# Performance work log

Hardware: AMD Instinct MI355X
Metric: run time of the kernel (lower is better)

## Reference

```python
import jax, jax.numpy as jnp
import numpy as np

B_, S_, F_ = 4096, 512, 3
MAT_PTS = 128
N_OUT = 3
N_LAT = MAT_PTS * N_OUT  # 384
E, NU = 3130.0, 0.3
A_H, B_H, C_H = 64.8, 33.6, 0.003407
MU = E / (2.0 * (1.0 + NU))
LAM = E * NU / ((1.0 + NU) * (1.0 - 2.0 * NU))
NEWTON_ITERS = 12
VEC1 = jnp.array([1.0, 1.0, 1.0, 0.0], dtype=jnp.float32)  # identity in Voigt-4 (xx,yy,zz,xy)


def setup_inputs() -> dict:
    key = jax.random.key(0)
    k1, k2, k3 = jax.random.split(key, 3)
    x = jax.random.normal(k1, (B_, S_, F_), dtype=jnp.float32) * 0.01
    W1 = jax.random.normal(k2, (N_LAT, F_), dtype=jnp.float32) * (1.0 / np.sqrt(F_))
    W2 = jax.random.normal(k3, (N_OUT, N_LAT), dtype=jnp.float32) * (1.0 / np.sqrt(N_LAT))
    return {"x": x, "W1": W1, "W2": W2}


def _j2_update(state, eps):
    """J2 plane-strain return mapping with exponential hardening.
    state: (ep [N,4] tensorial plastic strain, kappa [N] eq. plastic strain)
    eps:   [N,3] engineering strain (exx, eyy, gxy).
    Returns new state and stress [N,3] (sxx, syy, sxy)."""
    ep, kappa = state
    e = jnp.stack([eps[:, 0], eps[:, 1], jnp.zeros_like(eps[:, 0]), 0.5 * eps[:, 2]], axis=-1)
    ee = e - ep                                   # elastic strain, tensorial
    tr = ee[:, 0] + ee[:, 1] + ee[:, 2]
    sig = 2.0 * MU * ee + LAM * tr[:, None] * VEC1  # trial stress (xx,yy,zz,xy)
    p = (sig[:, 0] + sig[:, 1] + sig[:, 2]) / 3.0
    s = sig - p[:, None] * VEC1                    # deviatoric
    q = jnp.sqrt(1.5 * (s[:, 0] ** 2 + s[:, 1] ** 2 + s[:, 2] ** 2 + 2.0 * s[:, 3] ** 2))
    sy = A_H - B_H * jnp.exp(-kappa / C_H)
    f = q - sy                                     # yield function (trial)

    def newton_step(dg, _):
        kp = kappa + dg
        r = q - 3.0 * MU * dg - (A_H - B_H * jnp.exp(-kp / C_H))
        dr = -3.0 * MU - (B_H / C_H) * jnp.exp(-kp / C_H)
        dg_new = jnp.maximum(dg - r / dr, 0.0)
        return dg_new, None

    dg0 = jnp.zeros_like(q)
    dg, _ = jax.lax.scan(newton_step, dg0, None, length=NEWTON_ITERS)
    dg = jnp.where(f > 0.0, dg, 0.0)
    q_safe = jnp.maximum(q, 1e-12)
    n = 1.5 * s / q_safe[:, None]                  # flow direction
    sig_new = sig - 2.0 * MU * dg[:, None] * n
    ep_new = ep + dg[:, None] * n
    kappa_new = kappa + dg
    stress = jnp.stack([sig_new[:, 0], sig_new[:, 1], sig_new[:, 3]], axis=-1)
    return (ep_new, kappa_new), stress


def _forward(x, W1, W2):
    B, S, F = x.shape
    N = B * MAT_PTS  # material points across the batch
    # fc1 is time-independent: apply to all timesteps at once
    h = jnp.einsum('bsf,lf->bsl', x, W1)                 # [B,S,n_latents]
    eps_seq = h.reshape(B, S, MAT_PTS, F_).transpose(1, 0, 2, 3).reshape(S, N, F_)
    ep0 = jnp.zeros((N, 4), dtype=x.dtype)
    k0 = jnp.zeros((N,), dtype=x.dtype)
    _, stresses = jax.lax.scan(_j2_update, (ep0, k0), eps_seq)  # [S,N,3]
    lat = stresses.reshape(S, B, N_LAT).transpose(1, 0, 2)      # [B,S,n_latents]
    return jnp.einsum('bsl,ol->bso', lat, W2)                   # [B,S,n_outputs]


def reference(x, W1, W2):
    return _forward(x, W1, W2)
```

## Files before the change

kernel.cpp:

```cpp
#include <hip/hip_runtime.h>
#include <math.h>

#define S_LEN 512
#define CH 8
#define NSEG 128
#define TBL_L0 -22.0f
#define TBL_INVH 4.0f
#define TBL_H 0.25f

typedef float v2f __attribute__((ext_vector_type(2)));

__device__ __forceinline__ float fast_rcp(float x) { return __builtin_amdgcn_rcpf(x); }
__device__ __forceinline__ float fast_rsq(float x) { return __builtin_amdgcn_rsqf(x); }
__device__ __forceinline__ float exp2s(float x)    { return __builtin_amdgcn_exp2f(x); }
__device__ __forceinline__ v2f rsqv(v2f a)  { return (v2f){fast_rsq(a.x), fast_rsq(a.y)}; }
__device__ __forceinline__ v2f minv(v2f a, v2f b) { return __builtin_elementwise_min(a, b); }
__device__ __forceinline__ v2f vfma(v2f a, v2f b, v2f c) {
    return (v2f){ __builtin_fmaf(a.x, b.x, c.x), __builtin_fmaf(a.y, b.y, c.y) };
}

template <int CTRL>
__device__ __forceinline__ float dpp_add(float v) {
    int vi = __builtin_bit_cast(int, v);
    int t  = __builtin_amdgcn_update_dpp(vi, vi, CTRL, 0xF, 0xF, true);
    return v + __builtin_bit_cast(float, t);
}

__global__ __launch_bounds__(128, 4) void prnn_kernel(
    const float* __restrict__ x,
    const float* __restrict__ W1,
    const float* __restrict__ W2,
    float* __restrict__ out)
{
    const double MUd = 3130.0 / 2.6;
    const double Cd  = 0.003407;
    const double K2d = 1.4426950408889634 / Cd;
    const double S3  = 1.7320508075688772;
    const float MU      = (float)MUd;
    const float MUS3    = (float)(MUd * S3);
    const float CP      = (float)(7825.0 / 3.0);
    const float AH      = 64.8f;
    const float TMC     = (float)(3.0 * MUd * Cd);
    const float MQ      = (float)(-K2d / (3.0 * MUd));
    const float KA0     = (float)(1.4492898 + (64.8 / (3.0 * MUd)) * K2d);
    const float I3      = (float)(1.0 / 3.0);
    const float IS3     = (float)(1.0 / S3);
    const float LOG2E   = 1.4426950408889634f;
    const float LN08    = (float)(0.8 * 0.6931471805599453);

    const int tid  = threadIdx.x;
    const int lane = tid & 63;
    const int wv   = tid >> 6;
    const int b    = blockIdx.x * 2 + wv;

    __shared__ float2 xs01[2][S_LEN];
    __shared__ float  xs2g[2][S_LEN];
    __shared__ float  part[2][CH][3][17];
    __shared__ float2 wtab[NSEG];

    {
        float wn = 0.0f;
        if (tid <= NSEG) {
            const float sarg = TBL_L0 + (float)tid * TBL_H;
            const float z = exp2s(sarg);
            float w = fmaxf(LN08 * sarg, z * (1.0f - z));
            #pragma unroll
            for (int it = 0; it < 4; ++it) {
                const float y   = exp2s(w * LOG2E);
                const float g   = w * y;
                const float F   = g - z;
                const float Fp  = g + y;
                const float den = Fp*Fp - 0.5f*((F*y)*(2.0f + w));
                w = w - (F*Fp)*fast_rcp(den);
            }
            wn = w;
            ((float*)wtab)[tid] = wn;
        }
        __syncthreads();
        float wnext = 0.0f;
        if (tid < NSEG) wnext = ((float*)wtab)[tid + 1];
        __syncthreads();
        if (tid < NSEG) {
            const float sl = -TMC * (wnext - wn) * TBL_INVH;
            const float bi = (AH - TMC * wn) - sl * (TBL_L0 + (float)tid * TBL_H);
            wtab[tid] = (float2){sl, bi};
        }
        __syncthreads();
    }

    v2f P[3], Mr[3], T3[3], pv[3];
    #pragma unroll
    for (int f = 0; f < 3; ++f) {
        const int mA = lane, mB = lane + 64;
        v2f av = (v2f){ W1[(mA*3 + 0)*3 + f], W1[(mB*3 + 0)*3 + f] };
        v2f bv = (v2f){ W1[(mA*3 + 1)*3 + f], W1[(mB*3 + 1)*3 + f] };
        v2f cv = (v2f){ W1[(mA*3 + 2)*3 + f], W1[(mB*3 + 2)*3 + f] };
        P[f]  = MU*(av + bv);
        Mr[f] = MUS3*(av - bv);
        T3[f] = MUS3*cv;
        pv[f] = CP*(av + bv);
    }
    v2f wp[3], wm[3], w3[3];
    float w2raw[2][3][2];
    float gsel0, gsel1, gsel2;
    {
        float G[3][3];
        #pragma unroll
        for (int o = 0; o < 3; ++o) {
            v2f w0 = (v2f){ W2[o*384 + lane*3 + 0], W2[o*384 + (lane+64)*3 + 0] };
            v2f w1 = (v2f){ W2[o*384 + lane*3 + 1], W2[o*384 + (lane+64)*3 + 1] };
            v2f wsh= (v2f){ W2[o*384 + lane*3 + 2], W2[o*384 + (lane+64)*3 + 2] };
            wp[o] = I3 *(w0 + w1);
            wm[o] = IS3*(w0 - w1);
            w3[o] = IS3*wsh;
            v2f ws = w0 + w1;
            #pragma unroll
            for (int f = 0; f < 3; ++f) {
                v2f gv = ws * pv[f];
                float g = gv.x + gv.y;
                #pragma unroll
                for (int mm = 1; mm < 64; mm <<= 1) g += __shfl_xor(g, mm, 64);
                G[o][f] = g;
            }
        }
        const int ro = lane % 3;
        gsel0 = (ro == 0) ? G[0][0] : (ro == 1) ? G[1][0] : G[2][0];
        gsel1 = (ro == 0) ? G[0][1] : (ro == 1) ? G[1][1] : G[2][1];
        gsel2 = (ro == 0) ? G[0][2] : (ro == 1) ? G[1][2] : G[2][2];
    }

    const float* xb = x + (size_t)b * (S_LEN*3);
    for (int i = lane; i < S_LEN; i += 64) {
        const float c0 = xb[i*3 + 0], c1 = xb[i*3 + 1], c2 = xb[i*3 + 2];
        float p0 = 0.f, p1 = 0.f, p2 = 0.f;
        if (i > 0) { p0 = xb[i*3 - 3]; p1 = xb[i*3 - 2]; p2 = xb[i*3 - 1]; }
        xs01[wv][i] = (float2){ c0 - p0, c1 - p1 };
        xs2g[wv][i] = c2 - p2;
    }

    v2f sp = (v2f){0.f,0.f}, sm = sp, s3 = sp;
    v2f ka2 = (v2f){KA0, KA0};
    float* outb = out + (size_t)b * (S_LEN*3);
    const int rtt0 = (lane < 24) ? (lane / 3) : 0;

    #pragma unroll 1
    for (int tc = 0; tc < S_LEN; tc += CH) {
        const float* xrow = xb + (size_t)(tc + rtt0)*3;
        const float fx0 = xrow[0], fx1 = xrow[1], fx2 = xrow[2];

        #pragma unroll
        for (int tt = 0; tt < CH; ++tt) {
            const int t = tc + tt;
            const float2 dx01 = xs01[wv][t];
            const float  dx2  = xs2g[wv][t];
            const float dx0 = dx01.x, dx1 = dx01.y;

            v2f p  = P[0]*dx0 + P[1]*dx1 + P[2]*dx2 + sp;
            v2f m  = Mr[0]*dx0 + Mr[1]*dx1 + Mr[2]*dx2 + sm;
            v2f d3 = T3[0]*dx0 + T3[1]*dx1 + T3[2]*dx2 + s3;

            v2f h = vfma(p, p, vfma(m, m, vfma(d3, d3, (v2f){1e-24f,1e-24f})));
            v2f qi = rsqv(h);
            v2f q  = h * qi;

            v2f g   = q * MQ;
            v2f l2z = g + ka2;
            const float fix = __builtin_fmaf(l2z.x, TBL_INVH, -TBL_L0*TBL_INVH);
            const float fiy = __builtin_fmaf(l2z.y, TBL_INVH, -TBL_L0*TBL_INVH);
            const unsigned ix = (unsigned)fix;
            const unsigned iy = (unsigned)fiy;
            const float2 tx = wtab[ix];
            const float2 ty = wtab[iy];
            v2f sv = (v2f){ __builtin_fmaf(tx.x, l2z.x, tx.y),
                            __builtin_fmaf(ty.x, l2z.y, ty.y) };
            v2f u   = minv(sv*qi, (v2f){1.0f,1.0f});
            ka2 = vfma(-u, g, l2z);

            sp = u*p; sm = u*m; s3 = u*d3;

            v2f a0 = wp[0]*sp + wm[0]*sm + w3[0]*s3;
            v2f a1 = wp[1]*sp + wm[1]*sm + w3[1]*s3;
            v2f a2 = wp[2]*sp + wm[2]*sm + w3[2]*s3;
            float c0 = a0.x + a0.y;
            float c1 = a1.x + a1.y;
            float c2 = a2.x + a2.y;

            c0 = dpp_add<0xB1>(c0); c0 = dpp_add<0x4E>(c0);
            c1 = dpp_add<0xB1>(c1); c1 = dpp_add<0x4E>(c1);
            c2 = dpp_add<0xB1>(c2); c2 = dpp_add<0x4E>(c2);
            if ((lane & 3) == 0) {
                const int g16 = lane >> 2;
                part[wv][tt][0][g16] = c0;
                part[wv][tt][1][g16] = c1;
                part[wv][tt][2][g16] = c2;
            }
        }
        if (lane < 24) {
            const int rtt = lane / 3, ro = lane - rtt*3;
            const float4* pp = (const float4*)&part[wv][rtt][ro][0];
            const float4 v0 = pp[0], v1 = pp[1], v2v = pp[2], v3 = pp[3];
            float s = ((v0.x + v0.y) + (v0.z + v0.w))
                    + ((v1.x + v1.y) + (v1.z + v1.w))
                    + ((v2v.x + v2v.y) + (v2v.z + v2v.w))
                    + ((v3.x + v3.y) + (v3.z + v3.w));
            s = __builtin_fmaf(gsel0, fx0, s);
            s = __builtin_fmaf(gsel1, fx1, s);
            s = __builtin_fmaf(gsel2, fx2, s);
            outb[tc*3 + lane] = s;
        }
    }
}

extern "C" void kernel_launch(void* const* d_in, const int* in_sizes, int n_in,
                              void* d_out, int out_size, void* d_ws, size_t ws_size,
                              hipStream_t stream) {
    const float* x  = (const float*)d_in[0];
    const float* W1 = (const float*)d_in[1];
    const float* W2 = (const float*)d_in[2];
    float* out = (float*)d_out;
    prnn_kernel<<<2048, 128, 0, stream>>>(x, W1, W2, out);
}
```

Before: 275.5 us.

## Split each batch across two waves, one material point per lane

Before, each wave handled one batch element with two material points per lane. Now a 128-thread block handles one batch element, one point per thread, across 4096 blocks. The two waves' partial reductions are combined through shared memory with block barriers every chunk of timesteps. The lookup table is shrunk and shifted, and launch bounds are raised to allow more resident blocks. This halves the serial per-lane work and doubles parallelism, but adds two __syncthreads per chunk and loses the two-point ILP per lane.

```diff
diff --git a/kernel.cpp b/kernel.cpp
--- a/kernel.cpp
+++ b/kernel.cpp
@@ -3,21 +3,14 @@
 
 #define S_LEN 512
 #define CH 8
-#define NSEG 128
-#define TBL_L0 -22.0f
+#define NSEG 97
+#define TBL_L0 -15.0f
 #define TBL_INVH 4.0f
 #define TBL_H 0.25f
-
-typedef float v2f __attribute__((ext_vector_type(2)));
 
 __device__ __forceinline__ float fast_rcp(float x) { return __builtin_amdgcn_rcpf(x); }
 __device__ __forceinline__ float fast_rsq(float x) { return __builtin_amdgcn_rsqf(x); }
 __device__ __forceinline__ float exp2s(float x)    { return __builtin_amdgcn_exp2f(x); }
-__device__ __forceinline__ v2f rsqv(v2f a)  { return (v2f){fast_rsq(a.x), fast_rsq(a.y)}; }
-__device__ __forceinline__ v2f minv(v2f a, v2f b) { return __builtin_elementwise_min(a, b); }
-__device__ __forceinline__ v2f vfma(v2f a, v2f b, v2f c) {
-    return (v2f){ __builtin_fmaf(a.x, b.x, c.x), __builtin_fmaf(a.y, b.y, c.y) };
-}
 
 template <int CTRL>
 __device__ __forceinline__ float dpp_add(float v) {
@@ -26,7 +19,7 @@
     return v + __builtin_bit_cast(float, t);
 }
 
-__global__ __launch_bounds__(128, 4) void prnn_kernel(
+__global__ __launch_bounds__(128, 6) void prnn_kernel(
     const float* __restrict__ x,
     const float* __restrict__ W1,
     const float* __restrict__ W2,
@@ -51,11 +44,11 @@
     const int tid  = threadIdx.x;
     const int lane = tid & 63;
     const int wv   = tid >> 6;
-    const int b    = blockIdx.x * 2 + wv;
-
-    __shared__ float2 xs01[2][S_LEN];
-    __shared__ float  xs2g[2][S_LEN];
-    __shared__ float  part[2][CH][3][17];
+    const int b    = blockIdx.x;
+
+    __shared__ float2 xs01[S_LEN];
+    __shared__ float  xs2g[S_LEN];
+    __shared__ float  part[2][CH][3][16];
     __shared__ float2 wtab[NSEG];
 
     {
@@ -85,105 +78,111 @@
             const float bi = (AH - TMC * wn) - sl * (TBL_L0 + (float)tid * TBL_H);
             wtab[tid] = (float2){sl, bi};
         }
-        __syncthreads();
-    }
-
-    v2f P[3], Mr[3], T3[3], pv[3];
+    }
+
+    float P[3], Mr[3], T3[3], pvr[3];
     #pragma unroll
     for (int f = 0; f < 3; ++f) {
-        const int mA = lane, mB = lane + 64;
-        v2f av = (v2f){ W1[(mA*3 + 0)*3 + f], W1[(mB*3 + 0)*3 + f] };
-        v2f bv = (v2f){ W1[(mA*3 + 1)*3 + f], W1[(mB*3 + 1)*3 + f] };
-        v2f cv = (v2f){ W1[(mA*3 + 2)*3 + f], W1[(mB*3 + 2)*3 + f] };
-        P[f]  = MU*(av + bv);
-        Mr[f] = MUS3*(av - bv);
-        T3[f] = MUS3*cv;
-        pv[f] = CP*(av + bv);
-    }
-    v2f wp[3], wm[3], w3[3];
-    float w2raw[2][3][2];
-    float gsel0, gsel1, gsel2;
+        const float av = W1[(tid*3 + 0)*3 + f];
+        const float bv = W1[(tid*3 + 1)*3 + f];
+        const float cv = W1[(tid*3 + 2)*3 + f];
+        P[f]   = MU*(av + bv);
+        Mr[f]  = MUS3*(av - bv);
+        T3[f]  = MUS3*cv;
+        pvr[f] = CP*(av + bv);
+    }
+    float wp[3], wm[3], w3[3], ws[3];
+    #pragma unroll
+    for (int o = 0; o < 3; ++o) {
+        const float w0  = W2[o*384 + tid*3 + 0];
+        const float w1  = W2[o*384 + tid*3 + 1];
+        const float wsh = W2[o*384 + tid*3 + 2];
+        wp[o] = I3 *(w0 + w1);
+        wm[o] = IS3*(w0 - w1);
+        w3[o] = IS3*wsh;
+        ws[o] = w0 + w1;
+    }
+
+    float gsel0 = 0.f, gsel1 = 0.f, gsel2 = 0.f;
     {
-        float G[3][3];
         #pragma unroll
-        for (int o = 0; o < 3; ++o) {
-            v2f w0 = (v2f){ W2[o*384 + lane*3 + 0], W2[o*384 + (lane+64)*3 + 0] };
-            v2f w1 = (v2f){ W2[o*384 + lane*3 + 1], W2[o*384 + (lane+64)*3 + 1] };
-            v2f wsh= (v2f){ W2[o*384 + lane*3 + 2], W2[o*384 + (lane+64)*3 + 2] };
-            wp[o] = I3 *(w0 + w1);
-            wm[o] = IS3*(w0 - w1);
-            w3[o] = IS3*wsh;
-            v2f ws = w0 + w1;
+        for (int o = 0; o < 3; ++o)
             #pragma unroll
             for (int f = 0; f < 3; ++f) {
-                v2f gv = ws * pv[f];
-                float g = gv.x + gv.y;
+                float g = ws[o] * pvr[f];
                 #pragma unroll
                 for (int mm = 1; mm < 64; mm <<= 1) g += __shfl_xor(g, mm, 64);
-                G[o][f] = g;
-            }
-        }
-        const int ro = lane % 3;
-        gsel0 = (ro == 0) ? G[0][0] : (ro == 1) ? G[1][0] : G[2][0];
-        gsel1 = (ro == 0) ? G[0][1] : (ro == 1) ? G[1][1] : G[2][1];
-        gsel2 = (ro == 0) ? G[0][2] : (ro == 1) ? G[1][2] : G[2][2];
+                if (lane == 0) part[wv][0][o][f] = g;
+            }
+        __syncthreads();
+        if (tid < 24) {
+            const int ro = tid % 3;
+            gsel0 = part[0][0][ro][0] + part[1][0][ro][0];
+            gsel1 = part[0][0][ro][1] + part[1][0][ro][1];
+            gsel2 = part[0][0][ro][2] + part[1][0][ro][2];
+        }
+        __syncthreads();
     }
 
     const float* xb = x + (size_t)b * (S_LEN*3);
-    for (int i = lane; i < S_LEN; i += 64) {
+    for (int i = tid; i < S_LEN; i += 128) {
         const float c0 = xb[i*3 + 0], c1 = xb[i*3 + 1], c2 = xb[i*3 + 2];
         float p0 = 0.f, p1 = 0.f, p2 = 0.f;
         if (i > 0) { p0 = xb[i*3 - 3]; p1 = xb[i*3 - 2]; p2 = xb[i*3 - 1]; }
-        xs01[wv][i] = (float2){ c0 - p0, c1 - p1 };
-        xs2g[wv][i] = c2 - p2;
-    }
-
-    v2f sp = (v2f){0.f,0.f}, sm = sp, s3 = sp;
-    v2f ka2 = (v2f){KA0, KA0};
+        xs01[i] = (float2){ c0 - p0, c1 - p1 };
+        xs2g[i] = c2 - p2;
+    }
+    __syncthreads();
+
+    float sp = 0.f, sm = 0.f, s3 = 0.f, ka2 = KA0;
     float* outb = out + (size_t)b * (S_LEN*3);
-    const int rtt0 = (lane < 24) ? (lane / 3) : 0;
+    const int rtt0 = (tid < 24) ? (tid / 3) : 0;
 
     #pragma unroll 1
     for (int tc = 0; tc < S_LEN; tc += CH) {
-        const float* xrow = xb + (size_t)(tc + rtt0)*3;
-        const float fx0 = xrow[0], fx1 = xrow[1], fx2 = xrow[2];
+        float fx0 = 0.f, fx1 = 0.f, fx2 = 0.f;
+        if (tid < 24) {
+            const float* xrow = xb + (size_t)(tc + rtt0)*3;
+            fx0 = xrow[0]; fx1 = xrow[1]; fx2 = xrow[2];
+        }
 
         #pragma unroll
         for (int tt = 0; tt < CH; ++tt) {
             const int t = tc + tt;
-            const float2 dx01 = xs01[wv][t];
-            const float  dx2  = xs2g[wv][t];
+            const float2 dx01 = xs01[t];
+            const float  dx2  = xs2g[t];
             const float dx0 = dx01.x, dx1 = dx01.y;
 
-            v2f p  = P[0]*dx0 + P[1]*dx1 + P[2]*dx2 + sp;
-            v2f m  = Mr[0]*dx0 + Mr[1]*dx1 + Mr[2]*dx2 + sm;
-            v2f d3 = T3[0]*dx0 + T3[1]*dx1 + T3[2]*dx2 + s3;
-
-            v2f h = vfma(p, p, vfma(m, m, vfma(d3, d3, (v2f){1e-24f,1e-24f})));
-            v2f qi = rsqv(h);
-            v2f q  = h * qi;
-
-            v2f g   = q * MQ;
-            v2f l2z = g + ka2;
-            const float fix = __builtin_fmaf(l2z.x, TBL_INVH, -TBL_L0*TBL_INVH);
-            const float fiy = __builtin_fmaf(l2z.y, TBL_INVH, -TBL_L0*TBL_INVH);
-            const unsigned ix = (unsigned)fix;
-            const unsigned iy = (unsigned)fiy;
-            const float2 tx = wtab[ix];
-            const float2 ty = wtab[iy];
-            v2f sv = (v2f){ __builtin_fmaf(tx.x, l2z.x, tx.y),
-                            __builtin_fmaf(ty.x, l2z.y, ty.y) };
-            v2f u   = minv(sv*qi, (v2f){1.0f,1.0f});
-            ka2 = vfma(-u, g, l2z);
+            const float p  = __builtin_fmaf(P[0], dx0,
+                              __builtin_fmaf(P[1], dx1,
+                              __builtin_fmaf(P[2], dx2, sp)));
+            const float m  = __builtin_fmaf(Mr[0], dx0,
+                              __builtin_fmaf(Mr[1], dx1,
+                              __builtin_fmaf(Mr[2], dx2, sm)));
+            const float d3 = __builtin_fmaf(T3[0], dx0,
+                              __builtin_fmaf(T3[1], dx1,
+                              __builtin_fmaf(T3[2], dx2, s3)));
+
+            const float h  = __builtin_fmaf(p, p,
+                              __builtin_fmaf(m, m,
+                              __builtin_fmaf(d3, d3, 1e-24f)));
+            const float qi = fast_rsq(h);
+            const float q  = h * qi;
+
+            const float g   = q * MQ;
+            const float l2z = g + ka2;
+            const float fi  = __builtin_fmaf(l2z, TBL_INVH, -TBL_L0*TBL_INVH);
+            const unsigned ii = (unsigned)fi;
+            const float2 tb = wtab[ii];
+            const float sv  = __builtin_fmaf(tb.x, l2z, tb.y);
+            const float u   = fminf(sv*qi, 1.0f);
+            ka2 = __builtin_fmaf(-u, g, l2z);
 
             sp = u*p; sm = u*m; s3 = u*d3;
 
-            v2f a0 = wp[0]*sp + wm[0]*sm + w3[0]*s3;
-            v2f a1 = wp[1]*sp + wm[1]*sm + w3[1]*s3;
-            v2f a2 = wp[2]*sp + wm[2]*sm + w3[2]*s3;
-            float c0 = a0.x + a0.y;
-            float c1 = a1.x + a1.y;
-            float c2 = a2.x + a2.y;
+            float c0 = __builtin_fmaf(wp[0], sp, __builtin_fmaf(wm[0], sm, w3[0]*s3));
+            float c1 = __builtin_fmaf(wp[1], sp, __builtin_fmaf(wm[1], sm, w3[1]*s3));
+            float c2 = __builtin_fmaf(wp[2], sp, __builtin_fmaf(wm[2], sm, w3[2]*s3));
 
             c0 = dpp_add<0xB1>(c0); c0 = dpp_add<0x4E>(c0);
             c1 = dpp_add<0xB1>(c1); c1 = dpp_add<0x4E>(c1);
@@ -195,19 +194,24 @@
                 part[wv][tt][2][g16] = c2;
             }
         }
-        if (lane < 24) {
-            const int rtt = lane / 3, ro = lane - rtt*3;
-            const float4* pp = (const float4*)&part[wv][rtt][ro][0];
-            const float4 v0 = pp[0], v1 = pp[1], v2v = pp[2], v3 = pp[3];
-            float s = ((v0.x + v0.y) + (v0.z + v0.w))
-                    + ((v1.x + v1.y) + (v1.z + v1.w))
-                    + ((v2v.x + v2v.y) + (v2v.z + v2v.w))
-                    + ((v3.x + v3.y) + (v3.z + v3.w));
+        __syncthreads();
+        if (tid < 24) {
+            const int rtt = tid / 3, ro = tid - rtt*3;
+            const float4* p0 = (const float4*)&part[0][rtt][ro][0];
+            const float4* p1 = (const float4*)&part[1][rtt][ro][0];
+            float s = 0.0f;
+            #pragma unroll
+            for (int k = 0; k < 4; ++k) {
+                const float4 va = p0[k], vb = p1[k];
+                s += ((va.x + va.y) + (va.z + va.w))
+                   + ((vb.x + vb.y) + (vb.z + vb.w));
+            }
             s = __builtin_fmaf(gsel0, fx0, s);
             s = __builtin_fmaf(gsel1, fx1, s);
             s = __builtin_fmaf(gsel2, fx2, s);
-            outb[tc*3 + lane] = s;
-        }
+            outb[tc*3 + tid] = s;
+        }
+        __syncthreads();
     }
 }
 
@@ -218,5 +222,5 @@
     const float* W1 = (const float*)d_in[1];
     const float* W2 = (const float*)d_in[2];
     float* out = (float*)d_out;
-    prnn_kernel<<<2048, 128, 0, stream>>>(x, W1, W2, out);
+    prnn_kernel<<<4096, 128, 0, stream>>>(x, W1, W2, out);
 }
```

After: 339.6 us. +23.3%, slower.
